# Performance work log

Measured on AMD Instinct MI355X. Metric: run time of the kernel, lower is better.

The kernel has to match this reference:

```python
import jax, jax.numpy as jnp
from jax import lax
import numpy as np

NEG = -1e30


def setup_inputs() -> dict:
    key = jax.random.key(0)
    k0, k1, k2, k3 = jax.random.split(key, 4)
    B, txt_T, mel_T, n_mel = 32, 256, 2048, 80
    mu_logvar = jax.random.normal(k0, (B, txt_T, 2 * n_mel), jnp.float32)
    melspec = jax.random.normal(k1, (B, n_mel, mel_T), jnp.float32)
    text_lengths = jax.random.randint(k2, (B,), txt_T // 2, txt_T + 1)
    mel_lengths = jax.random.randint(k3, (B,), mel_T // 2, mel_T + 1)
    return dict(mu_logvar=mu_logvar, melspec=melspec,
                text_lengths=text_lengths, mel_lengths=mel_lengths)


def _log_prob_matrix(mu_logvar, melspec):
    # Gaussian log-prob (mean over mel channels), expanded into GEMM form:
    # -0.5/n_mel * sum_c [ (x_c - mu_c)^2 * exp(-logvar_c) + logvar_c ]
    n_mel = melspec.shape[1]
    mu = mu_logvar[..., :n_mel]           # [B, txt_T, C]
    logvar = mu_logvar[..., n_mel:]       # [B, txt_T, C]
    x = jnp.swapaxes(melspec, 1, 2)       # [B, mel_T, C]
    inv_var = jnp.exp(-logvar)
    t1 = jnp.einsum('btc,bjc->bjt', x * x, inv_var)        # sum x^2/var
    t2 = jnp.einsum('btc,bjc->bjt', x, mu * inv_var)       # sum x*mu/var
    t3 = jnp.sum(mu * mu * inv_var, axis=-1)               # [B, txt_T]
    t4 = jnp.sum(logvar, axis=-1)                          # [B, txt_T]
    return -0.5 * (t1 - 2.0 * t2 + (t3 + t4)[:, :, None]) / n_mel  # [B, txt_T, mel_T]


def _mdn_loss(mu_logvar, melspec, text_lengths, mel_lengths):
    log_prob = _log_prob_matrix(mu_logvar, melspec)   # [B, txt_T, mel_T]
    B, txt_T, mel_T = log_prob.shape
    col0 = jnp.full((B, txt_T), NEG, log_prob.dtype).at[:, 0].set(log_prob[:, 0, 0])

    def step(col, lp_t):
        shifted = jnp.concatenate([jnp.full((B, 1), NEG, col.dtype), col[:, :-1]], axis=1)
        new = jnp.logaddexp(col, shifted) + lp_t
        return new, new

    lp_rest = jnp.moveaxis(log_prob[:, :, 1:], 2, 0)  # [mel_T-1, B, txt_T]
    _, cols = lax.scan(step, col0, lp_rest)
    log_alpha = jnp.concatenate([col0[None], cols], axis=0)  # [mel_T, B, txt_T]

    b = jnp.arange(B)
    alpha_last = log_alpha[mel_lengths - 1, b, text_lengths - 1]
    alpha_last = alpha_last / mel_lengths.astype(log_prob.dtype)
    return -alpha_last.mean(), log_prob


def reference(mu_logvar, melspec, text_lengths, mel_lengths):
    mdn_loss, log_prob_matrix = _mdn_loss(mu_logvar, melspec, text_lengths, mel_lengths)
    return mdn_loss, log_prob_matrix
```

## Files before the change

kernel.cpp:

```cpp
#include <hip/hip_runtime.h>
#include <cstddef>
#include <cstdint>

#define NEGV -1e30f

constexpr int B_    = 32;
constexpr int TXT   = 256;
constexpr int MEL   = 2048;
constexpr int NMEL  = 80;

#define INV_LN2 1.4426950408889634f
#define LN2     0.6931471805599453f
#define M_DEAD  (-(1 << 30))

typedef float f32x4 __attribute__((ext_vector_type(4)));

__device__ __forceinline__ float wave_ror1_f(float x) {
    int xi = __float_as_int(x);
    int r  = __builtin_amdgcn_update_dpp(xi, xi, 0x13C , 0xF, 0xF, false);
    return __int_as_float(r);
}
__device__ __forceinline__ int wave_ror1_i(int x) {
    return __builtin_amdgcn_update_dpp(x, x, 0x13C , 0xF, 0xF, false);
}

__device__ __forceinline__ float exp2_nat(float x) {
#if __has_builtin(__builtin_amdgcn_exp2f)
    return __builtin_amdgcn_exp2f(x);
#else
    float r; asm("v_exp_f32 %0, %1" : "=v"(r) : "v"(x)); return r;
#endif
}
__device__ __forceinline__ float log2_nat(float x) {
#if __has_builtin(__builtin_amdgcn_logf)
    return __builtin_amdgcn_logf(x);
#else
    float r; asm("v_log_f32 %0, %1" : "=v"(r) : "v"(x)); return r;
#endif
}
__device__ __forceinline__ float ldexp_nat(float x, int n) {
#if __has_builtin(__builtin_amdgcn_ldexpf)
    return __builtin_amdgcn_ldexpf(x, n);
#else
    float r; asm("v_ldexp_f32 %0, %1, %2" : "=v"(r) : "v"(x), "v"(n)); return r;
#endif
}

__global__ __launch_bounds__(256) void precompute_kernel(
    const float* __restrict__ mu_logvar,
    float* __restrict__ IV, float* __restrict__ M2, float* __restrict__ S)
{
    const int b = blockIdx.x;
    const int j = threadIdx.x;
    const float* row = mu_logvar + (size_t)(b * TXT + j) * (2 * NMEL);
    float s = 0.f;
    for (int c = 0; c < NMEL; ++c) {
        float mu = row[c];
        float lv = row[NMEL + c];
        float iv = expf(-lv);
        IV[(b * NMEL + c) * TXT + j] = iv;
        M2[(b * NMEL + c) * TXT + j] = 2.0f * mu * iv;
        s += mu * mu * iv + lv;
    }
    S[b * TXT + j] = s;
}

__global__ __launch_bounds__(256) void logprob_kernel(
    const float* __restrict__ mel,
    const float* __restrict__ IV, const float* __restrict__ M2,
    const float* __restrict__ S,
    float* __restrict__ out1,
    float* __restrict__ lpT,
    int write_lpT)
{
    const int tt0 = blockIdx.x * 128;
    const int j0  = blockIdx.y * 64;
    const int b   = blockIdx.z;
    const int tx  = threadIdx.x & 15;
    const int ty  = threadIdx.x >> 4;

    __shared__ union SM {
        struct { float IV[NMEL][64]; float M2[NMEL][64]; } stage;
        float V[64][132];
    } sm;

    for (int idx = threadIdx.x; idx < NMEL * 64; idx += 256) {
        int c  = idx >> 6;
        int jj = idx & 63;
        sm.stage.IV[c][jj] = IV[(b * NMEL + c) * TXT + j0 + jj];
        sm.stage.M2[c][jj] = M2[(b * NMEL + c) * TXT + j0 + jj];
    }
    __syncthreads();

    float acc[4][8];
#pragma unroll
    for (int a = 0; a < 4; ++a)
#pragma unroll
        for (int d = 0; d < 8; ++d) acc[a][d] = 0.f;

    const float* melb = mel + (size_t)b * NMEL * MEL + tt0 + tx;

#pragma unroll 2
    for (int c = 0; c < NMEL; ++c) {
        float x[8];
#pragma unroll
        for (int d = 0; d < 8; ++d) x[d] = melb[(size_t)c * MEL + 16 * d];
        float4 iv = *(const float4*)&sm.stage.IV[c][ty * 4];
        float4 m2 = *(const float4*)&sm.stage.M2[c][ty * 4];
        float ivr[4] = {iv.x, iv.y, iv.z, iv.w};
        float m2r[4] = {m2.x, m2.y, m2.z, m2.w};
#pragma unroll
        for (int a = 0; a < 4; ++a) {
#pragma unroll
            for (int d = 0; d < 8; ++d) {
                float tmp = fmaf(ivr[a], x[d], -m2r[a]);
                acc[a][d] = fmaf(tmp, x[d], acc[a][d]);
            }
        }
    }

    const float c0 = -0.5f / (float)NMEL;
    float4 sj = *(const float4*)&S[b * TXT + j0 + ty * 4];
    float sjr[4] = {sj.x, sj.y, sj.z, sj.w};

    __syncthreads();
#pragma unroll
    for (int a = 0; a < 4; ++a) {
        const int jl = ty * 4 + a;
#pragma unroll
        for (int d = 0; d < 8; ++d) {
            sm.V[jl][tx + 16 * d] = c0 * (acc[a][d] + sjr[a]);
        }
    }
    __syncthreads();

    const int tid = threadIdx.x;

    {
        const int t4 = (tid & 31) * 4;
        const int jb = tid >> 5;
#pragma unroll
        for (int k = 0; k < 8; ++k) {
            const int jl = jb + 8 * k;
            float4 v = *(const float4*)&sm.V[jl][t4];
            *(float4*)&out1[(size_t)(b * TXT + j0 + jl) * MEL + tt0 + t4] = v;
        }
    }

    if (write_lpT) {
        const int j4 = (tid & 15) * 4;
        const int tb = tid >> 4;
#pragma unroll
        for (int k = 0; k < 8; ++k) {
            const int tl = tb + 16 * k;
            float4 v;
            v.x = exp2_nat(sm.V[j4 + 0][tl] * INV_LN2);
            v.y = exp2_nat(sm.V[j4 + 1][tl] * INV_LN2);
            v.z = exp2_nat(sm.V[j4 + 2][tl] * INV_LN2);
            v.w = exp2_nat(sm.V[j4 + 3][tl] * INV_LN2);
            *(float4*)&lpT[((size_t)b * MEL + tt0 + tl) * TXT + j0 + j4] = v;
        }
    }
}

__global__ __launch_bounds__(64, 1) void dp_kernel(
    const float* __restrict__ lpT,
    const int* __restrict__ tlen, const int* __restrict__ mlen,
    float* __restrict__ alpha)
{
    const int b = blockIdx.x;
    const int l = threadIdx.x;

    const int tl   = tlen[b];
    const int ml   = mlen[b];
    const int tmax = ml - 1;
    const int jt   = tl - 1;
    const float out_scale = LN2 / (float)ml;

    const float* sbase = lpT + (size_t)b * MEL * TXT;
    const bool z = (l == 0);

    __shared__ float ring[32][256];

    f32x4 ld0 = *(const f32x4*)(sbase + l * 4);
    int   ex0 = (int)(__float_as_uint(ld0[0]) >> 23) - 126;
    float q0n = ldexp_nat(ld0[0], -ex0);
    float q0 = z ? q0n : 0.f;
    float q1 = 0.f, q2 = 0.f, q3 = 0.f;
    int   M  = z ? ex0 : M_DEAD;

    if (tmax <= 0) {
        if (l == (jt >> 2)) {
            float vv = (jt == 0) ? log2_nat(ld0[0]) : NEGV;
            alpha[b] = vv * out_scale;
        }
        return;
    }

    __builtin_amdgcn_sched_barrier(0);

#define ISSUE(R)                                                              \
    __builtin_amdgcn_global_load_lds(                                         \
        (const __attribute__((address_space(1))) void*)(sbase + (size_t)(R) * TXT + l * 4), \
        (__attribute__((address_space(3))) void*)&ring[(R) & 31][0],          \
        16, 0, 0)

#pragma unroll
    for (int r = 1; r <= 16; ++r) ISSUE(r);

    asm volatile("s_waitcnt vmcnt(12)" ::: "memory");
    __builtin_amdgcn_sched_barrier(0);
    f32x4 cur0 = *(const f32x4*)&ring[1][l * 4];
    f32x4 cur1 = *(const f32x4*)&ring[2][l * 4];
    f32x4 cur2 = *(const f32x4*)&ring[3][l * 4];
    f32x4 cur3 = *(const f32x4*)&ring[4][l * 4];

#define DP_CORE(P)                                             \
    {                                                          \
        float qb = wave_ror1_f(q3);                            \
        int   Mb = wave_ror1_i(M);                             \
        qb = z ? 0.f : qb;                                     \
        int Mc  = (M > Mb) ? M : Mb;                           \
        int dql = M - Mc;                                      \
        int dqb = Mb - Mc;                                     \
        float qbs = ldexp_nat(qb, dqb);                        \
        float a0 = ldexp_nat(q0, dql);                         \
        float a1 = ldexp_nat(q1, dql);                         \
        float a2 = ldexp_nat(q2, dql);                         \
        float a3 = ldexp_nat(q3, dql);                         \
        q0 = (a0 + qbs) * (P)[0];                              \
        q1 = (a1 + a0)  * (P)[1];                              \
        q2 = (a2 + a1)  * (P)[2];                              \
        q3 = (a3 + a2)  * (P)[3];                              \
        M = Mc;                                                \
    }

#define RENORM()                                               \
    {                                                          \
        float mloc = fmaxf(fmaxf(q0, q1), fmaxf(q2, q3));      \
        int ex = (int)(__float_as_uint(mloc) >> 23) - 126;     \
        int nex = -ex;                                         \
        q0 = ldexp_nat(q0, nex);                               \
        q1 = ldexp_nat(q1, nex);                               \
        q2 = ldexp_nat(q2, nex);                               \
        q3 = ldexp_nat(q3, nex);                               \
        M = (mloc > 0.f) ? (M + ex) : M_DEAD;                  \
    }

    int t = 1;
    for (; t + 7 <= tmax; t += 4) {
        ISSUE(t + 16); ISSUE(t + 17); ISSUE(t + 18); ISSUE(t + 19);
        asm volatile("s_waitcnt vmcnt(12)" ::: "memory");
        __builtin_amdgcn_sched_barrier(0);
        f32x4 n0v = *(const f32x4*)&ring[(t + 4) & 31][l * 4];
        f32x4 n1v = *(const f32x4*)&ring[(t + 5) & 31][l * 4];
        f32x4 n2v = *(const f32x4*)&ring[(t + 6) & 31][l * 4];
        f32x4 n3v = *(const f32x4*)&ring[(t + 7) & 31][l * 4];
        DP_CORE(cur0); DP_CORE(cur1); DP_CORE(cur2); DP_CORE(cur3);
        RENORM();
        cur0 = n0v; cur1 = n1v; cur2 = n2v; cur3 = n3v;
    }

    asm volatile("s_waitcnt vmcnt(0)" ::: "memory");
    __builtin_amdgcn_sched_barrier(0);

    DP_CORE(cur0);
    if (t + 1 <= tmax) DP_CORE(cur1);
    if (t + 2 <= tmax) DP_CORE(cur2);
    if (t + 3 <= tmax) DP_CORE(cur3);
    RENORM();
#pragma unroll
    for (int k = 4; k <= 6; ++k) {
        if (t + k <= tmax) {
            f32x4 rr = *(const f32x4*)&ring[(t + k) & 31][l * 4];
            DP_CORE(rr);
        }
    }

#undef RENORM
#undef DP_CORE
#undef ISSUE

    const int lf = jt >> 2;
    const int ef = jt & 3;
    float v = (ef == 0) ? q0 : (ef == 1) ? q1 : (ef == 2) ? q2 : q3;
    if (l == lf) alpha[b] = (log2_nat(v) + (float)M) * out_scale;
}

__global__ __launch_bounds__(256) void dp_kernel_fallback(
    const float* __restrict__ lp,
    const int* __restrict__ tlen, const int* __restrict__ mlen,
    float* __restrict__ alpha)
{
    const int b    = blockIdx.x;
    const int j    = threadIdx.x;
    const int lane = j & 63;
    const int w    = j >> 6;

    const int tl   = tlen[b];
    const int ml   = mlen[b];
    const int tmax = ml - 1;
    const int jt   = tl - 1;
    const float inv_ml = 1.0f / (float)ml;

    __shared__ float bnd[2][4];
    if (threadIdx.x < 8) bnd[threadIdx.x >> 2][threadIdx.x & 3] = NEGV;
    __syncthreads();

    float cur = (j == 0) ? lp[(size_t)(b * TXT) * MEL] : NEGV;
    if (tmax == 0) {
        if (j == jt) alpha[b] = cur * inv_ml;
        return;
    }
    int p = 0;
    for (int t = 1; t <= tmax; ++t) {
        float lpc = lp[((size_t)(b * TXT + j)) * MEL + t];
        float sh = __shfl_up(cur, 1);
        if (lane == 0) sh = (w > 0) ? bnd[p][w - 1] : NEGV;
        float mx = fmaxf(cur, sh);
        float dd = fminf(cur, sh) - mx;
        float nv = mx + __logf(1.0f + __expf(dd)) + lpc;
        if (lane == 63) bnd[p ^ 1][w] = nv;
        if (t == tmax && j == jt) alpha[b] = nv * inv_ml;
        cur = nv;
        __syncthreads();
        p ^= 1;
    }
}

__global__ void reduce_kernel(const float* __restrict__ alpha, float* __restrict__ out)
{
    const int tid = threadIdx.x;
    float v = (tid < B_) ? alpha[tid] : 0.f;
#pragma unroll
    for (int m = 16; m >= 1; m >>= 1) v += __shfl_xor(v, m);
    if (tid == 0) out[0] = -v / (float)B_;
}

extern "C" void kernel_launch(void* const* d_in, const int* in_sizes, int n_in,
                              void* d_out, int out_size, void* d_ws, size_t ws_size,
                              hipStream_t stream)
{
    const float* mu_logvar = (const float*)d_in[0];
    const float* melspec   = (const float*)d_in[1];
    const int*   tlen      = (const int*)d_in[2];
    const int*   mlen      = (const int*)d_in[3];
    float* out = (float*)d_out;
    float* ws  = (float*)d_ws;

    const size_t IV_OFF    = 0;
    const size_t M2_OFF    = 655360;
    const size_t S_OFF     = 1310720;
    const size_t ALPHA_OFF = 1318912;
    const size_t LPT_OFF   = 1318944;
    const size_t LPT_ELEMS = (size_t)B_ * MEL * TXT;
    const size_t LPT_PAD   = (size_t)16 * TXT;

    float* IV    = ws + IV_OFF;
    float* M2    = ws + M2_OFF;
    float* S     = ws + S_OFF;
    float* alpha = ws + ALPHA_OFF;
    float* lpT   = ws + LPT_OFF;

    const bool use_lpT = ws_size >= (LPT_OFF + LPT_ELEMS + LPT_PAD) * sizeof(float);

    precompute_kernel<<<dim3(B_), dim3(256), 0, stream>>>(mu_logvar, IV, M2, S);

    logprob_kernel<<<dim3(MEL / 128, TXT / 64, B_), dim3(256), 0, stream>>>(
        melspec, IV, M2, S, out + 1, lpT, use_lpT ? 1 : 0);

    if (use_lpT) {
        dp_kernel<<<dim3(B_), dim3(64), 0, stream>>>(lpT, tlen, mlen, alpha);
    } else {
        dp_kernel_fallback<<<dim3(B_), dim3(256), 0, stream>>>(out + 1, tlen, mlen, alpha);
    }

    reduce_kernel<<<dim3(1), dim3(64), 0, stream>>>(alpha, out);
}
```

Measured before the change: 315.2 us.

## Precompute 4-step transfer coefficients to collapse DP recurrence into super-steps

Adds a parallel coeff_kernel that composes four consecutive linear-domain DP steps into a 5-band transfer matrix per text position. The sequential DP kernel then advances four mel frames per iteration with one cross-lane shift and one renormalization, shortening the serial dependency chain. In exchange it writes and streams five times the per-step data through a larger LDS ring. The super-step kernel only runs if the workspace is large enough; otherwise it falls back to the old single-step kernel. Numerics change because products of up to four probabilities are formed before renormalizing, so underflow is possible.

```diff
diff --git a/kernel.cpp b/kernel.cpp
--- a/kernel.cpp
+++ b/kernel.cpp
@@ -9,6 +9,9 @@
 constexpr int MEL   = 2048;
 constexpr int NMEL  = 80;
 
+constexpr int NGROUPS = 511;
+constexpr int GSTRIDE = 520;
+
 #define INV_LN2 1.4426950408889634f
 #define LN2     0.6931471805599453f
 #define M_DEAD  (-(1 << 30))
@@ -21,9 +24,8 @@
     return __int_as_float(r);
 }
 __device__ __forceinline__ int wave_ror1_i(int x) {
-    return __builtin_amdgcn_update_dpp(x, x, 0x13C , 0xF, 0xF, false);
-}
-
+    return __builtin_amdgcn_update_dpp(x, x, 0x13C, 0xF, 0xF, false);
+}
 __device__ __forceinline__ float exp2_nat(float x) {
 #if __has_builtin(__builtin_amdgcn_exp2f)
     return __builtin_amdgcn_exp2f(x);
@@ -163,7 +165,190 @@
     }
 }
 
-__global__ __launch_bounds__(64, 1) void dp_kernel(
+__global__ __launch_bounds__(256) void coeff_kernel(
+    const float* __restrict__ lpT, float* __restrict__ coef)
+{
+    const int c = blockIdx.x;
+    const int b = blockIdx.y;
+    const int j = threadIdx.x;
+
+    __shared__ float sp[32][256];
+    const int r0 = 32 * c + 1;
+    const float* src = lpT + (size_t)b * MEL * TXT;
+    for (int idx = threadIdx.x; idx < 32 * 256; idx += 256) {
+        int row = idx >> 8;
+        int col = idx & 255;
+        sp[row][col] = src[(size_t)(r0 + row) * TXT + col];
+    }
+    __syncthreads();
+
+    const int jm1 = (j >= 1) ? j - 1 : 0;
+    const int jm2 = (j >= 2) ? j - 2 : 0;
+    const int jm3 = (j >= 3) ? j - 3 : 0;
+
+#pragma unroll 2
+    for (int gi = 0; gi < 8; ++gi) {
+        int g = 8 * c + gi;
+        if (g >= NGROUPS) break;
+        const float* P1 = sp[4 * gi + 0];
+        const float* P2 = sp[4 * gi + 1];
+        const float* P3 = sp[4 * gi + 2];
+        const float* P4 = sp[4 * gi + 3];
+        float p1_0 = P1[j], p1_1 = P1[jm1], p1_2 = P1[jm2], p1_3 = P1[jm3];
+        float p2_0 = P2[j], p2_1 = P2[jm1], p2_2 = P2[jm2];
+        float p3_0 = P3[j], p3_1 = P3[jm1];
+        float p4_0 = P4[j];
+        float A0 = p2_0 * p1_0, A1 = p2_0 * (p1_0 + p1_1), A2 = p2_0 * p1_1;
+        float B0 = p2_1 * p1_1, B1 = p2_1 * (p1_1 + p1_2), B2 = p2_1 * p1_2;
+        float D0 = p2_2 * p1_2, D1 = p2_2 * (p1_2 + p1_3), D2 = p2_2 * p1_3;
+        float E0 = p3_0 * A0, E1 = p3_0 * (A1 + B0), E2 = p3_0 * (A2 + B1), E3 = p3_0 * B2;
+        float F0 = p3_1 * B0, F1 = p3_1 * (B1 + D0), F2 = p3_1 * (B2 + D1), F3 = p3_1 * D2;
+        float* dst = coef + (((size_t)b * GSTRIDE + g) * 5) * 256 + j;
+        dst[0]    = p4_0 * E0;
+        dst[256]  = p4_0 * (E1 + F0);
+        dst[512]  = p4_0 * (E2 + F1);
+        dst[768]  = p4_0 * (E3 + F2);
+        dst[1024] = p4_0 * F3;
+    }
+}
+
+__global__ __launch_bounds__(64, 1) void dp_super_kernel(
+    const float* __restrict__ lpT,
+    const float* __restrict__ coef,
+    const int* __restrict__ tlen, const int* __restrict__ mlen,
+    float* __restrict__ alpha)
+{
+    const int b = blockIdx.x;
+    const int l = threadIdx.x;
+
+    const int tl   = tlen[b];
+    const int ml   = mlen[b];
+    const int tmax = ml - 1;
+    const int jt   = tl - 1;
+    const float out_scale = LN2 / (float)ml;
+
+    const float* sbase = lpT  + (size_t)b * MEL * TXT;
+    const float* cbase = coef + (size_t)b * GSTRIDE * 5 * 256;
+    const bool z = (l == 0);
+
+    __shared__ float ring[40][256];
+
+    f32x4 ld0 = *(const f32x4*)(sbase + l * 4);
+    int   ex0 = (int)(__float_as_uint(ld0[0]) >> 23) - 126;
+    float q0n = ldexp_nat(ld0[0], -ex0);
+    float q0 = z ? q0n : 0.f;
+    float q1 = 0.f, q2 = 0.f, q3 = 0.f;
+    int   M  = z ? ex0 : M_DEAD;
+
+    if (tmax <= 0) {
+        if (l == (jt >> 2)) {
+            float vv = (jt == 0) ? log2_nat(ld0[0]) : NEGV;
+            alpha[b] = vv * out_scale;
+        }
+        return;
+    }
+
+    __builtin_amdgcn_sched_barrier(0);
+
+    const int nss  = tmax >> 2;
+    const int tail = tmax & 3;
+
+#define ISSUE1(SRC, SLOT)                                                     \
+    __builtin_amdgcn_global_load_lds(                                         \
+        (const __attribute__((address_space(1))) void*)(SRC),                 \
+        (__attribute__((address_space(3))) void*)&ring[(SLOT)][0], 16, 0, 0)
+#define ISSUE5(S)                                                             \
+    {                                                                         \
+        const float* s_ = cbase + (size_t)(S) * (5 * 256) + l * 4;            \
+        const int sl_ = ((S) & 7) * 5;                                        \
+        ISSUE1(s_,        sl_ + 0); ISSUE1(s_ + 256,  sl_ + 1);               \
+        ISSUE1(s_ + 512,  sl_ + 2); ISSUE1(s_ + 768,  sl_ + 3);               \
+        ISSUE1(s_ + 1024, sl_ + 4);                                           \
+    }
+
+#pragma unroll
+    for (int s = 0; s < 7; ++s) ISSUE5(s);
+
+    for (int s = 0; s < nss; ++s) {
+        ISSUE5(s + 7);
+        asm volatile("s_waitcnt vmcnt(35)" ::: "memory");
+        __builtin_amdgcn_sched_barrier(0);
+        const int sl = (s & 7) * 5;
+        f32x4 C0 = *(const f32x4*)&ring[sl + 0][l * 4];
+        f32x4 C1 = *(const f32x4*)&ring[sl + 1][l * 4];
+        f32x4 C2 = *(const f32x4*)&ring[sl + 2][l * 4];
+        f32x4 C3 = *(const f32x4*)&ring[sl + 3][l * 4];
+        f32x4 C4 = *(const f32x4*)&ring[sl + 4][l * 4];
+
+        float bq0 = wave_ror1_f(q0), bq1 = wave_ror1_f(q1);
+        float bq2 = wave_ror1_f(q2), bq3 = wave_ror1_f(q3);
+        int   bM  = wave_ror1_i(M);
+
+        int dq   = z ? (-(1 << 28)) : (bM - M);
+        int sin_ = (dq < 0) ? dq  : 0;
+        int sown = (dq > 0) ? -dq : 0;
+        int mup  = (dq > 0) ? dq  : 0;
+
+        float a0 = ldexp_nat(q0, sown), a1 = ldexp_nat(q1, sown);
+        float a2 = ldexp_nat(q2, sown), a3 = ldexp_nat(q3, sown);
+        float b0 = ldexp_nat(bq0, sin_), b1 = ldexp_nat(bq1, sin_);
+        float b2 = ldexp_nat(bq2, sin_), b3 = ldexp_nat(bq3, sin_);
+
+        float y0 = fmaf(C1[0], b3, fmaf(C2[0], b2, fmaf(C3[0], b1, fmaf(C4[0], b0, C0[0] * a0))));
+        float y1 = fmaf(C2[1], b3, fmaf(C3[1], b2, fmaf(C4[1], b1, fmaf(C1[1], a0, C0[1] * a1))));
+        float y2 = fmaf(C3[2], b3, fmaf(C4[2], b2, fmaf(C1[2], a1, fmaf(C2[2], a0, C0[2] * a2))));
+        float y3 = fmaf(C4[3], b3, fmaf(C1[3], a2, fmaf(C2[3], a1, fmaf(C3[3], a0, C0[3] * a3))));
+
+        float mloc = fmaxf(fmaxf(y0, y1), fmaxf(y2, y3));
+        int ex  = (int)(__float_as_uint(mloc) >> 23) - 126;
+        int nex = -ex;
+        q0 = ldexp_nat(y0, nex); q1 = ldexp_nat(y1, nex);
+        q2 = ldexp_nat(y2, nex); q3 = ldexp_nat(y3, nex);
+        int Mn = M + mup + ex;
+        M = (mloc > 0.f) ? Mn : M_DEAD;
+    }
+
+    asm volatile("s_waitcnt vmcnt(0)" ::: "memory");
+    __builtin_amdgcn_sched_barrier(0);
+
+    {
+        const int t0 = 4 * nss + 1;
+        f32x4 pr0 = *(const f32x4*)(sbase + (size_t)(t0 + 0) * TXT + l * 4);
+        f32x4 pr1 = *(const f32x4*)(sbase + (size_t)(t0 + 1) * TXT + l * 4);
+        f32x4 pr2 = *(const f32x4*)(sbase + (size_t)(t0 + 2) * TXT + l * 4);
+
+#define STEP1(P)                                                   \
+    {                                                              \
+        float qb = wave_ror1_f(q3);                                \
+        int   Mb = wave_ror1_i(M);                                 \
+        int dq   = z ? (-(1 << 28)) : (Mb - M);                    \
+        int si   = (dq < 0) ? dq  : 0;                             \
+        int so   = (dq > 0) ? -dq : 0;                             \
+        int mu   = (dq > 0) ? dq  : 0;                             \
+        float a0 = ldexp_nat(q0, so), a1 = ldexp_nat(q1, so);      \
+        float a2 = ldexp_nat(q2, so), a3 = ldexp_nat(q3, so);      \
+        float bb = ldexp_nat(qb, si);                              \
+        q0 = (a0 + bb) * (P)[0];                                   \
+        q1 = (a1 + a0) * (P)[1];                                   \
+        q2 = (a2 + a1) * (P)[2];                                   \
+        q3 = (a3 + a2) * (P)[3];                                   \
+        M += mu;                                                   \
+    }
+        if (tail >= 1) STEP1(pr0);
+        if (tail >= 2) STEP1(pr1);
+        if (tail >= 3) STEP1(pr2);
+#undef STEP1
+    }
+#undef ISSUE5
+#undef ISSUE1
+
+    const int lf = jt >> 2;
+    const int ef = jt & 3;
+    float v = (ef == 0) ? q0 : (ef == 1) ? q1 : (ef == 2) ? q2 : q3;
+    if (l == lf) alpha[b] = (log2_nat(v) + (float)M) * out_scale;
+}
+
+__global__ __launch_bounds__(64, 1) void dp_lin_kernel(
     const float* __restrict__ lpT,
     const int* __restrict__ tlen, const int* __restrict__ mlen,
     float* __restrict__ alpha)
@@ -234,7 +419,6 @@
         q3 = (a3 + a2)  * (P)[3];                              \
         M = Mc;                                                \
     }
-
 #define RENORM()                                               \
     {                                                          \
         float mloc = fmaxf(fmaxf(q0, q1), fmaxf(q2, q3));      \
@@ -276,7 +460,6 @@
             DP_CORE(rr);
         }
     }
-
 #undef RENORM
 #undef DP_CORE
 #undef ISSUE
@@ -355,22 +538,29 @@
     const size_t LPT_OFF   = 1318944;
     const size_t LPT_ELEMS = (size_t)B_ * MEL * TXT;
     const size_t LPT_PAD   = (size_t)16 * TXT;
+    const size_t COEF_OFF  = LPT_OFF + LPT_ELEMS + LPT_PAD;
+    const size_t COEF_ELEMS = (size_t)B_ * GSTRIDE * 5 * 256;
 
     float* IV    = ws + IV_OFF;
     float* M2    = ws + M2_OFF;
     float* S     = ws + S_OFF;
     float* alpha = ws + ALPHA_OFF;
     float* lpT   = ws + LPT_OFF;
-
-    const bool use_lpT = ws_size >= (LPT_OFF + LPT_ELEMS + LPT_PAD) * sizeof(float);
+    float* coef  = ws + COEF_OFF;
+
+    const bool use_lpT  = ws_size >= (LPT_OFF + LPT_ELEMS + LPT_PAD) * sizeof(float);
+    const bool use_coef = ws_size >= (COEF_OFF + COEF_ELEMS) * sizeof(float);
 
     precompute_kernel<<<dim3(B_), dim3(256), 0, stream>>>(mu_logvar, IV, M2, S);
 
     logprob_kernel<<<dim3(MEL / 128, TXT / 64, B_), dim3(256), 0, stream>>>(
         melspec, IV, M2, S, out + 1, lpT, use_lpT ? 1 : 0);
 
-    if (use_lpT) {
-        dp_kernel<<<dim3(B_), dim3(64), 0, stream>>>(lpT, tlen, mlen, alpha);
+    if (use_coef) {
+        coeff_kernel<<<dim3(64, B_), dim3(256), 0, stream>>>(lpT, coef);
+        dp_super_kernel<<<dim3(B_), dim3(64), 0, stream>>>(lpT, coef, tlen, mlen, alpha);
+    } else if (use_lpT) {
+        dp_lin_kernel<<<dim3(B_), dim3(64), 0, stream>>>(lpT, tlen, mlen, alpha);
     } else {
         dp_kernel_fallback<<<dim3(B_), dim3(256), 0, stream>>>(out + 1, tlen, mlen, alpha);
     }
```

Result: no change. 311.7 us (-1.1%).
